# Kernel tuning notes

Measured on AMD Instinct MI355X. Metric: run time of the kernel, lower is better.

Reference implementation:

```python
import jax, jax.numpy as jnp
import numpy as np

D_MODEL = 1024
NUM_HEADS = 16
D_K = D_MODEL // NUM_HEADS
LOCAL_WINDOW = 3
STRIDE = 4


def strided_mask(seq_len):
    # position i attends to j iff j <= i and (i-j <= local_window or (i-j) % stride == 0)
    i = jnp.arange(seq_len)[:, None]
    j = jnp.arange(seq_len)[None, :]
    d = i - j
    return (d >= 0) & ((d <= LOCAL_WINDOW) | (d % STRIDE == 0))


def setup_inputs() -> dict:
    key = jax.random.key(0)
    ks = jax.random.split(key, 11)
    B, S, D = 4, 1024, D_MODEL
    s = 1.0 / np.sqrt(D)
    inp = {
        "Q": jax.random.normal(ks[0], (B, S, D), jnp.float32),
        "K": jax.random.normal(ks[1], (B, S, D), jnp.float32),
        "V": jax.random.normal(ks[2], (B, S, D), jnp.float32),
        "Wq": jax.random.normal(ks[3], (D, D), jnp.float32) * s,
        "bq": jnp.zeros((D,), jnp.float32),
        "Wk": jax.random.normal(ks[4], (D, D), jnp.float32) * s,
        "bk": jnp.zeros((D,), jnp.float32),
        "Wv": jax.random.normal(ks[5], (D, D), jnp.float32) * s,
        "bv": jnp.zeros((D,), jnp.float32),
        "Wo": jax.random.normal(ks[6], (D, D), jnp.float32) * s,
        "bo": jnp.zeros((D,), jnp.float32),
    }
    return inp


def reference(Q, K, V, Wq, bq, Wk, bk, Wv, bv, Wo, bo):
    B, S, D = Q.shape
    H, dk = NUM_HEADS, D_K

    def split(x):  # [B,S,D] -> [B,H,S,dk]
        return x.reshape(B, S, H, dk).transpose(0, 2, 1, 3)

    q = split(Q @ Wq + bq)
    k = split(K @ Wk + bk)
    v = split(V @ Wv + bv)

    scores = jnp.einsum("bhsd,bhtd->bhst", q, k) / jnp.sqrt(
        jnp.asarray(dk, jnp.float32))
    m = strided_mask(S)[None, None]  # [1,1,S,S]
    scores = jnp.where(m, scores, -1e9)
    attn = jax.nn.softmax(scores, axis=-1)
    out = jnp.einsum("bhst,bhtd->bhsd", attn, v)
    out = out.transpose(0, 2, 1, 3).reshape(B, S, D)  # combine heads
    return out @ Wo + bo
```

## Files before the change

### kernel.cpp

```cpp
#include <hip/hip_runtime.h>

typedef _Float16 f16;
typedef __attribute__((ext_vector_type(8))) _Float16 f16x8;
typedef __attribute__((ext_vector_type(4))) _Float16 f16x4;
typedef __attribute__((ext_vector_type(4))) float f32x4;

#define MFMA16(a, b, c) __builtin_amdgcn_mfma_f32_16x16x32_f16((a), (b), (c), 0, 0, 0)

__device__ __forceinline__ void gld_lds16(const void* g, void* l) {
  __builtin_amdgcn_global_load_lds(
      (__attribute__((address_space(1))) void*)const_cast<void*>(g),
      (__attribute__((address_space(3))) void*)l, 16, 0, 0);
}

__device__ __forceinline__ f16x8 ld8(const f16* p) { return *(const f16x8*)p; }

__global__ __launch_bounds__(256) void cvt_all_kernel(
    const float* __restrict__ Q, const float* __restrict__ K, const float* __restrict__ V,
    f16* __restrict__ oq, f16* __restrict__ ok, f16* __restrict__ ov,
    const float* __restrict__ Wq, const float* __restrict__ Wk,
    const float* __restrict__ Wv, const float* __restrict__ Wo,
    f16* __restrict__ Tq, f16* __restrict__ Tk, f16* __restrict__ Tv, f16* __restrict__ To) {
  __shared__ float tile[64][65];
  if (blockIdx.z < 3) {
    const float* src = blockIdx.z == 0 ? Q : (blockIdx.z == 1 ? K : V);
    f16* dst = blockIdx.z == 0 ? oq : (blockIdx.z == 1 ? ok : ov);
    size_t i = ((size_t)blockIdx.x * 256 + threadIdx.x) * 4;
    float4 f = *(const float4*)(src + i);
    f16x4 o4;
    o4.x = (f16)f.x; o4.y = (f16)f.y; o4.z = (f16)f.z; o4.w = (f16)f.w;
    *(f16x4*)(dst + i) = o4;
    return;
  }
  if (blockIdx.x >= 1024) return;
  const int zz = blockIdx.x >> 8;
  const float* W = zz == 0 ? Wq : (zz == 1 ? Wk : (zz == 2 ? Wv : Wo));
  f16* T = zz == 0 ? Tq : (zz == 1 ? Tk : (zz == 2 ? Tv : To));
  const int tidx = blockIdx.x & 255;
  const int k0 = (tidx & 15) * 64, n0 = (tidx >> 4) * 64;
  const int tx = threadIdx.x & 63, ty = threadIdx.x >> 6;
#pragma unroll
  for (int rr = 0; rr < 16; ++rr) {
    int r = rr * 4 + ty;
    tile[r][tx] = W[(size_t)(k0 + r) * 1024 + n0 + tx];
  }
  __syncthreads();
#pragma unroll
  for (int rr = 0; rr < 16; ++rr) {
    int nn = rr * 4 + ty;
    T[(size_t)(n0 + nn) * 1024 + k0 + tx] = (f16)tile[tx][nn];
  }
}

template <bool QKV>
__global__ __launch_bounds__(256) void gemm_bt_kernel(
    const f16* __restrict__ A0, const f16* __restrict__ A1, const f16* __restrict__ A2,
    const f16* __restrict__ B0, const f16* __restrict__ B1, const f16* __restrict__ B2,
    const float* __restrict__ bias0, const float* __restrict__ bias1, const float* __restrict__ bias2,
    f16* __restrict__ C0, f16* __restrict__ C1, f16* __restrict__ C2,
    f16* __restrict__ C3, float* __restrict__ Cf) {
  const int z = blockIdx.z;
  const f16* A = z == 0 ? A0 : (z == 1 ? A1 : A2);
  const f16* Bt = z == 0 ? B0 : (z == 1 ? B1 : B2);
  const float* bias = z == 0 ? bias0 : (z == 1 ? bias1 : bias2);

  __shared__ alignas(16) f16 lA[128 * 32];
  __shared__ alignas(16) f16 lB[128 * 32];

  const int t = threadIdx.x;
  const int w = t >> 6, lane = t & 63, quad = lane >> 4, l15 = lane & 15;
  const int wm = w >> 1, wn = w & 1;
  const int mbase = blockIdx.x * 128;
  const int nbase = blockIdx.y * 128;

  const f32x4 zero4 = {0.f, 0.f, 0.f, 0.f};
  f32x4 acc[4][4];
#pragma unroll
  for (int mi = 0; mi < 4; ++mi)
#pragma unroll
    for (int ni = 0; ni < 4; ++ni) acc[mi][ni] = zero4;

  const int r = t >> 2;
  const int koff = (t & 3) * 8;

  for (int k0 = 0; k0 < 1024; k0 += 32) {
    __syncthreads();
    gld_lds16(A + (size_t)(mbase + r) * 1024 + k0 + koff, (char*)lA + w * 1024);
    gld_lds16(A + (size_t)(mbase + 64 + r) * 1024 + k0 + koff, (char*)lA + 4096 + w * 1024);
    gld_lds16(Bt + (size_t)(nbase + r) * 1024 + k0 + koff, (char*)lB + w * 1024);
    gld_lds16(Bt + (size_t)(nbase + 64 + r) * 1024 + k0 + koff, (char*)lB + 4096 + w * 1024);
    __syncthreads();

    f16x8 af[4], bf[4];
#pragma unroll
    for (int mi = 0; mi < 4; ++mi)
      af[mi] = ld8(&lA[(wm * 64 + mi * 16 + l15) * 32 + quad * 8]);
#pragma unroll
    for (int ni = 0; ni < 4; ++ni)
      bf[ni] = ld8(&lB[(wn * 64 + ni * 16 + l15) * 32 + quad * 8]);
#pragma unroll
    for (int mi = 0; mi < 4; ++mi)
#pragma unroll
      for (int ni = 0; ni < 4; ++ni)
        acc[mi][ni] = MFMA16(af[mi], bf[ni], acc[mi][ni]);
  }

#pragma unroll
  for (int mi = 0; mi < 4; ++mi) {
#pragma unroll
    for (int ni = 0; ni < 4; ++ni) {
#pragma unroll
      for (int rg = 0; rg < 4; ++rg) {
        const int row = mbase + wm * 64 + mi * 16 + quad * 4 + rg;
        const int col = nbase + wn * 64 + ni * 16 + l15;
        const float v = acc[mi][ni][rg] + bias[col];
        if (QKV) {
          const int bh = (row >> 10) * 16 + (col >> 6);
          const int s = row & 1023, d = col & 63;
          const f16 hv = (f16)v;
          if (z != 2) {
            f16* Ch = (z == 0) ? C0 : C1;
            Ch[(size_t)bh * 65536 + s * 64 + d] = hv;
          } else {
            C2[(size_t)bh * 65536 + s * 64 + d] = hv;
            const int rr = s & 3, n = s >> 2, wi = n & 63;
            C3[(size_t)bh * 65536 + (size_t)rr * 16384 + (size_t)d * 256 +
               (n & ~63) + ((wi & 15) << 2) + (wi >> 4)] = hv;
          }
        } else {
          Cf[(size_t)row * 1024 + col] = v;
        }
      }
    }
  }
}

__global__ __launch_bounds__(256) void gemm_out_kernel(
    const f16* __restrict__ A, const f16* __restrict__ Bt,
    const float* __restrict__ bias, float* __restrict__ Cf) {
  __shared__ alignas(16) f16 lA[64 * 32];
  __shared__ alignas(16) f16 lB[128 * 32];

  const int t = threadIdx.x;
  const int w = t >> 6, lane = t & 63, quad = lane >> 4, l15 = lane & 15;
  const int wm = w >> 1, wn = w & 1;
  const int mbase = blockIdx.x * 64;
  const int nbase = blockIdx.y * 128;

  const f32x4 zero4 = {0.f, 0.f, 0.f, 0.f};
  f32x4 acc[2][4];
#pragma unroll
  for (int mi = 0; mi < 2; ++mi)
#pragma unroll
    for (int ni = 0; ni < 4; ++ni) acc[mi][ni] = zero4;

  const int r = t >> 2;
  const int koff = (t & 3) * 8;

  for (int k0 = 0; k0 < 1024; k0 += 32) {
    __syncthreads();
    gld_lds16(A + (size_t)(mbase + r) * 1024 + k0 + koff, (char*)lA + w * 1024);
    gld_lds16(Bt + (size_t)(nbase + r) * 1024 + k0 + koff, (char*)lB + w * 1024);
    gld_lds16(Bt + (size_t)(nbase + 64 + r) * 1024 + k0 + koff, (char*)lB + 4096 + w * 1024);
    __syncthreads();

    f16x8 af[2], bf[4];
#pragma unroll
    for (int mi = 0; mi < 2; ++mi)
      af[mi] = ld8(&lA[(wm * 32 + mi * 16 + l15) * 32 + quad * 8]);
#pragma unroll
    for (int ni = 0; ni < 4; ++ni)
      bf[ni] = ld8(&lB[(wn * 64 + ni * 16 + l15) * 32 + quad * 8]);
#pragma unroll
    for (int mi = 0; mi < 2; ++mi)
#pragma unroll
      for (int ni = 0; ni < 4; ++ni)
        acc[mi][ni] = MFMA16(af[mi], bf[ni], acc[mi][ni]);
  }

#pragma unroll
  for (int mi = 0; mi < 2; ++mi)
#pragma unroll
    for (int ni = 0; ni < 4; ++ni)
#pragma unroll
      for (int rg = 0; rg < 4; ++rg) {
        const int row = mbase + wm * 32 + mi * 16 + quad * 4 + rg;
        const int col = nbase + wn * 64 + ni * 16 + l15;
        Cf[(size_t)row * 1024 + col] = acc[mi][ni][rg] + bias[col];
      }
}

__global__ __launch_bounds__(256) void attn_fused_kernel(
    const f16* __restrict__ qh, const f16* __restrict__ kh,
    const f16* __restrict__ vtg, const f16* __restrict__ vh,
    f16* __restrict__ ao) {
  const int t = threadIdx.x;
  const int w = t >> 6, lane = t & 63, quad = lane >> 4, l15 = lane & 15;
  const int widx = blockIdx.x + 1024 * w;
  const int bh = (widx & 255) >> 2, r = widx & 3;
  const int wq = widx >> 8;
  const int m0 = wq * 16;
  const int ntiles = (wq >> 2) + 1;

  __shared__ alignas(16) f16 lp[4][16 * 72];

  const f16* qb = qh + (size_t)bh * 65536;
  const f16* kb = kh + (size_t)bh * 65536;
  const f16* vb = vtg + (size_t)bh * 65536 + (size_t)r * 16384;
  const float SCL2 = 0.125f * 1.44269504f;

  f16x8 aq[2];
  {
    const int i = 4 * (m0 + l15) + r;
#pragma unroll
    for (int ko = 0; ko < 2; ++ko)
      aq[ko] = ld8(qb + (size_t)i * 64 + ko * 32 + quad * 8);
  }

  const f32x4 zero4 = {0.f, 0.f, 0.f, 0.f};
  f32x4 o[4];
  float mrun[4], lrun[4];
#pragma unroll
  for (int i = 0; i < 4; ++i) {
    o[i] = zero4; mrun[i] = -1e30f; lrun[i] = 0.f;
  }

  for (int jt = 0; jt < ntiles; ++jt) {
    const int n0 = jt * 64;
    f16x8 bk0[4], bk1[4], bv0[4], bv1[4];
#pragma unroll
    for (int nt = 0; nt < 4; ++nt) {
      const f16* kr = kb + (size_t)(4 * (n0 + nt * 16 + l15) + r) * 64;
      bk0[nt] = ld8(kr + quad * 8);
      bk1[nt] = ld8(kr + 32 + quad * 8);
      const f16* vr = vb + (size_t)(nt * 16 + l15) * 256 + n0;
      bv0[nt] = ld8(vr + quad * 8);
      bv1[nt] = ld8(vr + 32 + quad * 8);
    }
    const bool lastt = (jt == ntiles - 1);
    f32x4 sc[4];
    __builtin_amdgcn_s_setprio(1);
#pragma unroll
    for (int nt = 0; nt < 4; ++nt) {
      f32x4 c = MFMA16(aq[0], bk0[nt], zero4);
      sc[nt] = MFMA16(aq[1], bk1[nt], c);
    }
    __builtin_amdgcn_s_setprio(0);
#pragma unroll
    for (int rg = 0; rg < 4; ++rg) {
      const int m = m0 + quad * 4 + rg;
      float s[4];
#pragma unroll
      for (int nt = 0; nt < 4; ++nt) {
        float vsc = sc[nt][rg] * SCL2;
        if (lastt) vsc = (n0 + nt * 16 + l15 <= m) ? vsc : -3.0e38f;
        s[nt] = vsc;
      }
      float tm = fmaxf(fmaxf(s[0], s[1]), fmaxf(s[2], s[3]));
      tm = fmaxf(tm, __shfl_xor(tm, 1));
      tm = fmaxf(tm, __shfl_xor(tm, 2));
      tm = fmaxf(tm, __shfl_xor(tm, 4));
      tm = fmaxf(tm, __shfl_xor(tm, 8));
      const float mnew = fmaxf(mrun[rg], tm);
      const float alpha = exp2f(mrun[rg] - mnew);
      float p[4], ps = 0.f;
#pragma unroll
      for (int nt = 0; nt < 4; ++nt) { p[nt] = exp2f(s[nt] - mnew); ps += p[nt]; }
      ps += __shfl_xor(ps, 1);
      ps += __shfl_xor(ps, 2);
      ps += __shfl_xor(ps, 4);
      ps += __shfl_xor(ps, 8);
      lrun[rg] = lrun[rg] * alpha + ps;
      mrun[rg] = mnew;
#pragma unroll
      for (int ntv = 0; ntv < 4; ++ntv) o[ntv][rg] *= alpha;
      f16x4 pk;
      pk.x = (f16)p[0]; pk.y = (f16)p[1]; pk.z = (f16)p[2]; pk.w = (f16)p[3];
      *(f16x4*)&lp[w][(quad * 4 + rg) * 72 + l15 * 4] = pk;
    }
    {
      const f16x8 ap0 = ld8(&lp[w][l15 * 72 + quad * 8]);
      const f16x8 ap1 = ld8(&lp[w][l15 * 72 + 32 + quad * 8]);
      __builtin_amdgcn_s_setprio(1);
#pragma unroll
      for (int ntv = 0; ntv < 4; ++ntv) {
        f32x4 c = MFMA16(ap0, bv0[ntv], o[ntv]);
        o[ntv] = MFMA16(ap1, bv1[ntv], c);
      }
      __builtin_amdgcn_s_setprio(0);
    }
  }

  float sd[3][4];
#pragma unroll
  for (int d = 1; d <= 3; ++d) {
    f16x8 bd0, bd1;
    {
      int j = 4 * (m0 + l15) + r - d;
      if (j < 0) j = 0;
      const f16* kr = kb + (size_t)j * 64;
      bd0 = ld8(kr + quad * 8);
      bd1 = ld8(kr + 32 + quad * 8);
    }
    f32x4 c = MFMA16(aq[0], bd0, zero4);
    c = MFMA16(aq[1], bd1, c);
#pragma unroll
    for (int rg = 0; rg < 4; ++rg) {
      const float dv = __shfl(c[rg], quad * 20 + rg);
      const int i = 4 * (m0 + quad * 4 + rg) + r;
      sd[d - 1][rg] = (i >= d) ? dv * SCL2 : -3.0e38f;
    }
  }

  const f16* vhb2 = vh + (size_t)bh * 65536;
  const int b = bh >> 4, h = bh & 15;
#pragma unroll
  for (int rg = 0; rg < 4; ++rg) {
    const int i = 4 * (m0 + quad * 4 + rg) + r;
    const float mdg = fmaxf(fmaxf(sd[0][rg], sd[1][rg]), sd[2][rg]);
    const float M = fmaxf(mrun[rg], mdg);
    const float fs = exp2f(mrun[rg] - M);
    float p[3];
    float ltot = lrun[rg] * fs;
#pragma unroll
    for (int d = 0; d < 3; ++d) { p[d] = exp2f(sd[d][rg] - M); ltot += p[d]; }
    const float inv = 1.0f / ltot;
    const f16* v1 = vhb2 + (size_t)((i >= 1) ? i - 1 : 0) * 64;
    const f16* v2 = vhb2 + (size_t)((i >= 2) ? i - 2 : 0) * 64;
    const f16* v3 = vhb2 + (size_t)((i >= 3) ? i - 3 : 0) * 64;
    f16* aor = ao + ((size_t)(b * 1024 + i)) * 1024 + h * 64;
#pragma unroll
    for (int ntv = 0; ntv < 4; ++ntv) {
      const int dc = ntv * 16 + l15;
      const float ov = p[0] * (float)v1[dc] + p[1] * (float)v2[dc] +
                       p[2] * (float)v3[dc];
      aor[dc] = (f16)((o[ntv][rg] * fs + ov) * inv);
    }
  }
}

extern "C" void kernel_launch(void* const* d_in, const int* in_sizes, int n_in,
                              void* d_out, int out_size, void* d_ws, size_t ws_size,
                              hipStream_t stream) {
  const float* Q = (const float*)d_in[0];
  const float* K = (const float*)d_in[1];
  const float* V = (const float*)d_in[2];
  const float* Wq = (const float*)d_in[3];
  const float* bq = (const float*)d_in[4];
  const float* Wk = (const float*)d_in[5];
  const float* bk = (const float*)d_in[6];
  const float* Wv = (const float*)d_in[7];
  const float* bv = (const float*)d_in[8];
  const float* Wo = (const float*)d_in[9];
  const float* bo = (const float*)d_in[10];
  float* out = (float*)d_out;

  char* ws = (char*)d_ws;
  const size_t MB = 1ull << 20;
  f16* Xq  = (f16*)(ws + 0 * MB);
  f16* Xk  = (f16*)(ws + 8 * MB);
  f16* Xv  = (f16*)(ws + 16 * MB);
  f16* TWq = (f16*)(ws + 24 * MB);
  f16* TWk = (f16*)(ws + 26 * MB);
  f16* TWv = (f16*)(ws + 28 * MB);
  f16* TWo = (f16*)(ws + 30 * MB);
  f16* qhb = (f16*)(ws + 32 * MB);
  f16* khb = (f16*)(ws + 40 * MB);
  f16* vhb = (f16*)(ws + 48 * MB);
  f16* vtg = (f16*)(ws + 56 * MB);
  f16* aob = (f16*)(ws + 17 * MB);

  cvt_all_kernel<<<dim3(4096, 1, 4), 256, 0, stream>>>(
      Q, K, V, Xq, Xk, Xv, Wq, Wk, Wv, Wo, TWq, TWk, TWv, TWo);
  gemm_bt_kernel<true><<<dim3(32, 8, 3), 256, 0, stream>>>(
      Xq, Xk, Xv, TWq, TWk, TWv, bq, bk, bv, qhb, khb, vhb, vtg, nullptr);
  attn_fused_kernel<<<dim3(1024), 256, 0, stream>>>(qhb, khb, vtg, vhb, aob);
  gemm_out_kernel<<<dim3(64, 8), 256, 0, stream>>>(aob, TWo, bo, out);
}
```

Baseline: 215.0 us.

## Enlarge QKV GEMM tiles to 256x256 with 4-stage swizzled LDS pipeline

The QKV projection GEMM now uses 512-thread blocks computing 256x256 output tiles. A 4-slot LDS ring buffer of 128 KB is filled by direct global-to-LDS loads issued three stages ahead, with explicit vmcnt waits, and an XOR swizzle on the LDS layout to cut bank conflicts. The intent is to hide global load latency and raise arithmetic intensity per block. The trade-offs are fewer blocks (192 versus 768) across 256 CUs, heavy LDS use that limits occupancy to one block per CU, and higher register pressure from 32 accumulators. The attention output buffer also moves to a workspace offset that no longer overlaps the input staging region.

```diff
diff --git a/kernel.cpp b/kernel.cpp
--- a/kernel.cpp
+++ b/kernel.cpp
@@ -53,7 +53,7 @@
 }
 
 template <bool QKV>
-__global__ __launch_bounds__(256) void gemm_bt_kernel(
+__global__ __launch_bounds__(512) void gemm_bt_kernel(
     const f16* __restrict__ A0, const f16* __restrict__ A1, const f16* __restrict__ A2,
     const f16* __restrict__ B0, const f16* __restrict__ B1, const f16* __restrict__ B2,
     const float* __restrict__ bias0, const float* __restrict__ bias1, const float* __restrict__ bias2,
@@ -64,54 +64,81 @@
   const f16* Bt = z == 0 ? B0 : (z == 1 ? B1 : B2);
   const float* bias = z == 0 ? bias0 : (z == 1 ? bias1 : bias2);
 
-  __shared__ alignas(16) f16 lA[128 * 32];
-  __shared__ alignas(16) f16 lB[128 * 32];
+  __shared__ alignas(16) char lds[131072];
 
   const int t = threadIdx.x;
   const int w = t >> 6, lane = t & 63, quad = lane >> 4, l15 = lane & 15;
-  const int wm = w >> 1, wn = w & 1;
-  const int mbase = blockIdx.x * 128;
-  const int nbase = blockIdx.y * 128;
+  const int wm = w >> 2, wn = w & 3;
+  const int mbase = blockIdx.x * 256;
+  const int nbase = blockIdx.y * 256;
 
   const f32x4 zero4 = {0.f, 0.f, 0.f, 0.f};
-  f32x4 acc[4][4];
-#pragma unroll
-  for (int mi = 0; mi < 4; ++mi)
+  f32x4 acc[8][4];
+#pragma unroll
+  for (int mi = 0; mi < 8; ++mi)
 #pragma unroll
     for (int ni = 0; ni < 4; ++ni) acc[mi][ni] = zero4;
 
-  const int r = t >> 2;
-  const int koff = (t & 3) * 8;
-
-  for (int k0 = 0; k0 < 1024; k0 += 32) {
-    __syncthreads();
-    gld_lds16(A + (size_t)(mbase + r) * 1024 + k0 + koff, (char*)lA + w * 1024);
-    gld_lds16(A + (size_t)(mbase + 64 + r) * 1024 + k0 + koff, (char*)lA + 4096 + w * 1024);
-    gld_lds16(Bt + (size_t)(nbase + r) * 1024 + k0 + koff, (char*)lB + w * 1024);
-    gld_lds16(Bt + (size_t)(nbase + 64 + r) * 1024 + k0 + koff, (char*)lB + 4096 + w * 1024);
-    __syncthreads();
-
-    f16x8 af[4], bf[4];
-#pragma unroll
-    for (int mi = 0; mi < 4; ++mi)
-      af[mi] = ld8(&lA[(wm * 64 + mi * 16 + l15) * 32 + quad * 8]);
+  const int srow = t >> 2;
+  const int koff = (((t & 3) ^ ((t >> 2) & 3) ^ ((t >> 4) & 3)) << 3);
+  const int woff = w << 10;
+
+#define STAGE256(slot, k0)                                                          \
+  do {                                                                              \
+    char* sb = lds + (slot) * 32768;                                                \
+    gld_lds16(A + (size_t)(mbase + srow) * 1024 + (k0) + koff, sb + woff);          \
+    gld_lds16(A + (size_t)(mbase + 128 + srow) * 1024 + (k0) + koff,                \
+              sb + 8192 + woff);                                                    \
+    gld_lds16(Bt + (size_t)(nbase + srow) * 1024 + (k0) + koff, sb + 16384 + woff); \
+    gld_lds16(Bt + (size_t)(nbase + 128 + srow) * 1024 + (k0) + koff,               \
+              sb + 24576 + woff);                                                   \
+  } while (0)
+
+  STAGE256(0, 0);
+  STAGE256(1, 32);
+  STAGE256(2, 64);
+
+  const int pos = ((quad ^ ((l15 & 3) ^ ((l15 >> 2) & 3))) << 3);
+
+  for (int tt = 0; tt < 32; ++tt) {
+    if (tt < 30)
+      asm volatile("s_waitcnt vmcnt(8)" ::: "memory");
+    else if (tt == 30)
+      asm volatile("s_waitcnt vmcnt(4)" ::: "memory");
+    else
+      asm volatile("s_waitcnt vmcnt(0)" ::: "memory");
+    __builtin_amdgcn_s_barrier();
+
+    const f16* sA = (const f16*)(lds + (tt & 3) * 32768);
+    const f16* sB = sA + 8192;
+    f16x8 af[8], bf[4];
+#pragma unroll
+    for (int mi = 0; mi < 8; ++mi)
+      af[mi] = ld8(&sA[(wm * 128 + mi * 16 + l15) * 32 + pos]);
 #pragma unroll
     for (int ni = 0; ni < 4; ++ni)
-      bf[ni] = ld8(&lB[(wn * 64 + ni * 16 + l15) * 32 + quad * 8]);
-#pragma unroll
-    for (int mi = 0; mi < 4; ++mi)
+      bf[ni] = ld8(&sB[(wn * 64 + ni * 16 + l15) * 32 + pos]);
+
+    __builtin_amdgcn_s_setprio(1);
+#pragma unroll
+    for (int mi = 0; mi < 8; ++mi)
 #pragma unroll
       for (int ni = 0; ni < 4; ++ni)
         acc[mi][ni] = MFMA16(af[mi], bf[ni], acc[mi][ni]);
-  }
-
-#pragma unroll
-  for (int mi = 0; mi < 4; ++mi) {
+    __builtin_amdgcn_s_setprio(0);
+
+    __builtin_amdgcn_s_barrier();
+    if (tt < 29) STAGE256((tt + 3) & 3, (tt + 3) * 32);
+  }
+#undef STAGE256
+
+#pragma unroll
+  for (int mi = 0; mi < 8; ++mi) {
 #pragma unroll
     for (int ni = 0; ni < 4; ++ni) {
 #pragma unroll
       for (int rg = 0; rg < 4; ++rg) {
-        const int row = mbase + wm * 64 + mi * 16 + quad * 4 + rg;
+        const int row = mbase + wm * 128 + mi * 16 + quad * 4 + rg;
         const int col = nbase + wn * 64 + ni * 16 + l15;
         const float v = acc[mi][ni][rg] + bias[col];
         if (QKV) {
@@ -368,11 +395,11 @@
   f16* khb = (f16*)(ws + 40 * MB);
   f16* vhb = (f16*)(ws + 48 * MB);
   f16* vtg = (f16*)(ws + 56 * MB);
-  f16* aob = (f16*)(ws + 17 * MB);
+  f16* aob = (f16*)(ws + 64 * MB);
 
   cvt_all_kernel<<<dim3(4096, 1, 4), 256, 0, stream>>>(
       Q, K, V, Xq, Xk, Xv, Wq, Wk, Wv, Wo, TWq, TWk, TWv, TWo);
-  gemm_bt_kernel<true><<<dim3(32, 8, 3), 256, 0, stream>>>(
+  gemm_bt_kernel<true><<<dim3(16, 4, 3), 512, 0, stream>>>(
       Xq, Xk, Xv, TWq, TWk, TWv, bq, bk, bv, qhb, khb, vhb, vtg, nullptr);
   attn_fused_kernel<<<dim3(1024), 256, 0, stream>>>(qhb, khb, vtg, vhb, aob);
   gemm_out_kernel<<<dim3(64, 8), 256, 0, stream>>>(aob, TWo, bo, out);
```

Measured after the change: 234.0 us. +8.8%, slower.

## Fuse fp32-to-fp16 activation conversion into QKV projection GEMM loads

Applied to the files above, without the earlier changes.

The separate pass that converts the Q, K and V activations to fp16 is removed. The QKV GEMM now loads fp32 activation tiles straight into LDS, using an XOR swizzle to limit bank conflicts, and converts them to fp16 in registers before the MFMA. This drops one full read and write of the 48 MB activations plus a kernel launch. In exchange each A tile moves twice as many bytes through global memory and LDS, and the fp32 LDS footprint grows.

```diff
diff --git a/kernel.cpp b/kernel.cpp
--- a/kernel.cpp
+++ b/kernel.cpp
@@ -15,29 +15,15 @@
 
 __device__ __forceinline__ f16x8 ld8(const f16* p) { return *(const f16x8*)p; }
 
-__global__ __launch_bounds__(256) void cvt_all_kernel(
-    const float* __restrict__ Q, const float* __restrict__ K, const float* __restrict__ V,
-    f16* __restrict__ oq, f16* __restrict__ ok, f16* __restrict__ ov,
+__global__ __launch_bounds__(256) void cvt_wT_kernel(
     const float* __restrict__ Wq, const float* __restrict__ Wk,
     const float* __restrict__ Wv, const float* __restrict__ Wo,
     f16* __restrict__ Tq, f16* __restrict__ Tk, f16* __restrict__ Tv, f16* __restrict__ To) {
+  const int z = blockIdx.z;
+  const float* W = z == 0 ? Wq : (z == 1 ? Wk : (z == 2 ? Wv : Wo));
+  f16* T = z == 0 ? Tq : (z == 1 ? Tk : (z == 2 ? Tv : To));
   __shared__ float tile[64][65];
-  if (blockIdx.z < 3) {
-    const float* src = blockIdx.z == 0 ? Q : (blockIdx.z == 1 ? K : V);
-    f16* dst = blockIdx.z == 0 ? oq : (blockIdx.z == 1 ? ok : ov);
-    size_t i = ((size_t)blockIdx.x * 256 + threadIdx.x) * 4;
-    float4 f = *(const float4*)(src + i);
-    f16x4 o4;
-    o4.x = (f16)f.x; o4.y = (f16)f.y; o4.z = (f16)f.z; o4.w = (f16)f.w;
-    *(f16x4*)(dst + i) = o4;
-    return;
-  }
-  if (blockIdx.x >= 1024) return;
-  const int zz = blockIdx.x >> 8;
-  const float* W = zz == 0 ? Wq : (zz == 1 ? Wk : (zz == 2 ? Wv : Wo));
-  f16* T = zz == 0 ? Tq : (zz == 1 ? Tk : (zz == 2 ? Tv : To));
-  const int tidx = blockIdx.x & 255;
-  const int k0 = (tidx & 15) * 64, n0 = (tidx >> 4) * 64;
+  const int k0 = blockIdx.x * 64, n0 = blockIdx.y * 64;
   const int tx = threadIdx.x & 63, ty = threadIdx.x >> 6;
 #pragma unroll
   for (int rr = 0; rr < 16; ++rr) {
@@ -54,17 +40,17 @@
 
 template <bool QKV>
 __global__ __launch_bounds__(256) void gemm_bt_kernel(
-    const f16* __restrict__ A0, const f16* __restrict__ A1, const f16* __restrict__ A2,
+    const float* __restrict__ A0, const float* __restrict__ A1, const float* __restrict__ A2,
     const f16* __restrict__ B0, const f16* __restrict__ B1, const f16* __restrict__ B2,
     const float* __restrict__ bias0, const float* __restrict__ bias1, const float* __restrict__ bias2,
     f16* __restrict__ C0, f16* __restrict__ C1, f16* __restrict__ C2,
     f16* __restrict__ C3, float* __restrict__ Cf) {
   const int z = blockIdx.z;
-  const f16* A = z == 0 ? A0 : (z == 1 ? A1 : A2);
+  const float* A = z == 0 ? A0 : (z == 1 ? A1 : A2);
   const f16* Bt = z == 0 ? B0 : (z == 1 ? B1 : B2);
   const float* bias = z == 0 ? bias0 : (z == 1 ? bias1 : bias2);
 
-  __shared__ alignas(16) f16 lA[128 * 32];
+  __shared__ alignas(16) float lAf[128 * 32];
   __shared__ alignas(16) f16 lB[128 * 32];
 
   const int t = threadIdx.x;
@@ -80,21 +66,33 @@
 #pragma unroll
     for (int ni = 0; ni < 4; ++ni) acc[mi][ni] = zero4;
 
-  const int r = t >> 2;
-  const int koff = (t & 3) * 8;
+  const int ra = t >> 3;
+  const int ka = (((t & 7) ^ ((t >> 3) & 7)) << 2);
+  const int rb = t >> 2;
+  const int kb = (t & 3) * 8;
+  const int xr = l15 & 7;
 
   for (int k0 = 0; k0 < 1024; k0 += 32) {
     __syncthreads();
-    gld_lds16(A + (size_t)(mbase + r) * 1024 + k0 + koff, (char*)lA + w * 1024);
-    gld_lds16(A + (size_t)(mbase + 64 + r) * 1024 + k0 + koff, (char*)lA + 4096 + w * 1024);
-    gld_lds16(Bt + (size_t)(nbase + r) * 1024 + k0 + koff, (char*)lB + w * 1024);
-    gld_lds16(Bt + (size_t)(nbase + 64 + r) * 1024 + k0 + koff, (char*)lB + 4096 + w * 1024);
+#pragma unroll
+    for (int c4 = 0; c4 < 4; ++c4)
+      gld_lds16(A + (size_t)(mbase + c4 * 32 + ra) * 1024 + k0 + ka,
+                (char*)lAf + c4 * 4096 + w * 1024);
+    gld_lds16(Bt + (size_t)(nbase + rb) * 1024 + k0 + kb, (char*)lB + w * 1024);
+    gld_lds16(Bt + (size_t)(nbase + 64 + rb) * 1024 + k0 + kb, (char*)lB + 4096 + w * 1024);
     __syncthreads();
 
     f16x8 af[4], bf[4];
 #pragma unroll
-    for (int mi = 0; mi < 4; ++mi)
-      af[mi] = ld8(&lA[(wm * 64 + mi * 16 + l15) * 32 + quad * 8]);
+    for (int mi = 0; mi < 4; ++mi) {
+      const float* rp = lAf + (wm * 64 + mi * 16 + l15) * 32;
+      const float4 u0 = *(const float4*)(rp + (((quad << 1) ^ xr) << 2));
+      const float4 u1 = *(const float4*)(rp + ((((quad << 1) | 1) ^ xr) << 2));
+      f16x8 a;
+      a[0] = (f16)u0.x; a[1] = (f16)u0.y; a[2] = (f16)u0.z; a[3] = (f16)u0.w;
+      a[4] = (f16)u1.x; a[5] = (f16)u1.y; a[6] = (f16)u1.z; a[7] = (f16)u1.w;
+      af[mi] = a;
+    }
 #pragma unroll
     for (int ni = 0; ni < 4; ++ni)
       bf[ni] = ld8(&lB[(wn * 64 + ni * 16 + l15) * 32 + quad * 8]);
@@ -357,9 +355,6 @@
 
   char* ws = (char*)d_ws;
   const size_t MB = 1ull << 20;
-  f16* Xq  = (f16*)(ws + 0 * MB);
-  f16* Xk  = (f16*)(ws + 8 * MB);
-  f16* Xv  = (f16*)(ws + 16 * MB);
   f16* TWq = (f16*)(ws + 24 * MB);
   f16* TWk = (f16*)(ws + 26 * MB);
   f16* TWv = (f16*)(ws + 28 * MB);
@@ -368,12 +363,12 @@
   f16* khb = (f16*)(ws + 40 * MB);
   f16* vhb = (f16*)(ws + 48 * MB);
   f16* vtg = (f16*)(ws + 56 * MB);
-  f16* aob = (f16*)(ws + 17 * MB);
-
-  cvt_all_kernel<<<dim3(4096, 1, 4), 256, 0, stream>>>(
-      Q, K, V, Xq, Xk, Xv, Wq, Wk, Wv, Wo, TWq, TWk, TWv, TWo);
+  f16* aob = (f16*)(ws + 0 * MB);
+
+  cvt_wT_kernel<<<dim3(16, 16, 4), 256, 0, stream>>>(
+      Wq, Wk, Wv, Wo, TWq, TWk, TWv, TWo);
   gemm_bt_kernel<true><<<dim3(32, 8, 3), 256, 0, stream>>>(
-      Xq, Xk, Xv, TWq, TWk, TWv, bq, bk, bv, qhb, khb, vhb, vtg, nullptr);
+      Q, K, V, TWq, TWk, TWv, bq, bk, bv, qhb, khb, vhb, vtg, nullptr);
   attn_fused_kernel<<<dim3(1024), 256, 0, stream>>>(qhb, khb, vtg, vhb, aob);
   gemm_out_kernel<<<dim3(64, 8), 256, 0, stream>>>(aob, TWo, bo, out);
 }
```

Result: slower. 231.6 us (+7.7%).

## Switch QKV GEMM to 32x32x16 MFMA with XOR-swizzled LDS layout

Applied to the files above, without the earlier changes.

The QKV projection GEMM now uses 32x32x16 MFMA instructions in place of 16x16x32, so each wave computes its 64x64 tile with four larger MFMAs per k-step. The global-to-LDS load offsets and the fragment reads use an XOR swizzle on the k chunk to avoid LDS bank conflicts. Fewer MFMA issues and fewer LDS fragment loads per FLOP are the aim, at the cost of a more complex epilogue index mapping. The attention output buffer is also moved to a non-overlapping workspace offset.

```diff
diff --git a/kernel.cpp b/kernel.cpp
--- a/kernel.cpp
+++ b/kernel.cpp
@@ -4,8 +4,10 @@
 typedef __attribute__((ext_vector_type(8))) _Float16 f16x8;
 typedef __attribute__((ext_vector_type(4))) _Float16 f16x4;
 typedef __attribute__((ext_vector_type(4))) float f32x4;
+typedef __attribute__((ext_vector_type(16))) float f32x16;
 
 #define MFMA16(a, b, c) __builtin_amdgcn_mfma_f32_16x16x32_f16((a), (b), (c), 0, 0, 0)
+#define MFMA32(a, b, c) __builtin_amdgcn_mfma_f32_32x32x16_f16((a), (b), (c), 0, 0, 0)
 
 __device__ __forceinline__ void gld_lds16(const void* g, void* l) {
   __builtin_amdgcn_global_load_lds(
@@ -68,20 +70,25 @@
   __shared__ alignas(16) f16 lB[128 * 32];
 
   const int t = threadIdx.x;
-  const int w = t >> 6, lane = t & 63, quad = lane >> 4, l15 = lane & 15;
+  const int w = t >> 6, lane = t & 63;
+  const int c31 = lane & 31, hi = lane >> 5;
   const int wm = w >> 1, wn = w & 1;
   const int mbase = blockIdx.x * 128;
   const int nbase = blockIdx.y * 128;
 
-  const f32x4 zero4 = {0.f, 0.f, 0.f, 0.f};
-  f32x4 acc[4][4];
-#pragma unroll
-  for (int mi = 0; mi < 4; ++mi)
-#pragma unroll
-    for (int ni = 0; ni < 4; ++ni) acc[mi][ni] = zero4;
+  f32x16 acc[2][2];
+#pragma unroll
+  for (int mi = 0; mi < 2; ++mi)
+#pragma unroll
+    for (int ni = 0; ni < 2; ++ni)
+#pragma unroll
+      for (int e = 0; e < 16; ++e) acc[mi][ni][e] = 0.f;
 
   const int r = t >> 2;
-  const int koff = (t & 3) * 8;
+  const int koff = (((t & 3) ^ (r & 3)) << 3);
+  const int xk = (c31 & 3);
+  const int abase = (wm * 64 + c31) * 32;
+  const int bbase = (wn * 64 + c31) * 32;
 
   for (int k0 = 0; k0 < 1024; k0 += 32) {
     __syncthreads();
@@ -91,28 +98,28 @@
     gld_lds16(Bt + (size_t)(nbase + 64 + r) * 1024 + k0 + koff, (char*)lB + 4096 + w * 1024);
     __syncthreads();
 
-    f16x8 af[4], bf[4];
-#pragma unroll
-    for (int mi = 0; mi < 4; ++mi)
-      af[mi] = ld8(&lA[(wm * 64 + mi * 16 + l15) * 32 + quad * 8]);
-#pragma unroll
-    for (int ni = 0; ni < 4; ++ni)
-      bf[ni] = ld8(&lB[(wn * 64 + ni * 16 + l15) * 32 + quad * 8]);
-#pragma unroll
-    for (int mi = 0; mi < 4; ++mi)
-#pragma unroll
-      for (int ni = 0; ni < 4; ++ni)
-        acc[mi][ni] = MFMA16(af[mi], bf[ni], acc[mi][ni]);
-  }
-
-#pragma unroll
-  for (int mi = 0; mi < 4; ++mi) {
-#pragma unroll
-    for (int ni = 0; ni < 4; ++ni) {
-#pragma unroll
-      for (int rg = 0; rg < 4; ++rg) {
-        const int row = mbase + wm * 64 + mi * 16 + quad * 4 + rg;
-        const int col = nbase + wn * 64 + ni * 16 + l15;
+#pragma unroll
+    for (int kk = 0; kk < 2; ++kk) {
+      const int pos = ((kk * 2 + hi) ^ xk) << 3;
+      const f16x8 a0 = ld8(&lA[abase + pos]);
+      const f16x8 a1 = ld8(&lA[abase + 32 * 32 + pos]);
+      const f16x8 b0 = ld8(&lB[bbase + pos]);
+      const f16x8 b1 = ld8(&lB[bbase + 32 * 32 + pos]);
+      acc[0][0] = MFMA32(a0, b0, acc[0][0]);
+      acc[0][1] = MFMA32(a0, b1, acc[0][1]);
+      acc[1][0] = MFMA32(a1, b0, acc[1][0]);
+      acc[1][1] = MFMA32(a1, b1, acc[1][1]);
+    }
+  }
+
+#pragma unroll
+  for (int mi = 0; mi < 2; ++mi) {
+#pragma unroll
+    for (int ni = 0; ni < 2; ++ni) {
+#pragma unroll
+      for (int rg = 0; rg < 16; ++rg) {
+        const int row = mbase + wm * 64 + mi * 32 + (rg & 3) + 8 * (rg >> 2) + 4 * hi;
+        const int col = nbase + wn * 64 + ni * 32 + c31;
         const float v = acc[mi][ni][rg] + bias[col];
         if (QKV) {
           const int bh = (row >> 10) * 16 + (col >> 6);
@@ -368,7 +375,7 @@
   f16* khb = (f16*)(ws + 40 * MB);
   f16* vhb = (f16*)(ws + 48 * MB);
   f16* vtg = (f16*)(ws + 56 * MB);
-  f16* aob = (f16*)(ws + 17 * MB);
+  f16* aob = (f16*)(ws + 64 * MB);
 
   cvt_all_kernel<<<dim3(4096, 1, 4), 256, 0, stream>>>(
       Q, K, V, Xq, Xk, Xv, Wq, Wk, Wv, Wo, TWq, TWk, TWv, TWo);
```

New measurement: 233.1 us. +8.4%, slower.
